# Optimization experiments

Measured on AMD Instinct MI355X. Metric: run time of the kernel, lower is better.

Reference implementation:

```python
import jax, jax.numpy as jnp
import numpy as np
from jax import lax

# shifts generated by _generate_shifts(kernel_size=3): (s1, s2) pairs with
# (s1, s2) >= (0, 0) lexicographically, excluding (0, 0)
SHIFTS = [(0, 1), (1, -1), (1, 0), (1, 1)]


def conv2d_same(x, w, b):
    # x: (B, C_in, H, W), w: (C_out, C_in, kH, kW), b: (C_out,)
    y = lax.conv_general_dilated(
        x, w, window_strides=(1, 1), padding='SAME',
        dimension_numbers=('NCHW', 'OIHW', 'NCHW'))
    return y + b[None, :, None, None]


def setup_inputs() -> dict:
    key = jax.random.key(0)
    k1, k2, k3, k4, k5 = jax.random.split(key, 5)
    B, C_in, C_out, H, W, K = 8, 64, 64, 256, 256, 3
    fan = C_in * K * K
    return {
        'x': jax.random.normal(k1, (B, C_in, H, W), dtype=jnp.float32),
        'w1': jax.random.normal(k2, (C_out, C_in, K, K), dtype=jnp.float32) / np.sqrt(fan),
        'b1': jax.random.normal(k3, (C_out,), dtype=jnp.float32) * 0.01,
        'w2': jax.random.normal(k4, (C_out, C_in, K, K), dtype=jnp.float32) / np.sqrt(fan),
        'b2': jax.random.normal(k5, (C_out,), dtype=jnp.float32) * 0.01,
    }


def reference(x, w1, b1, w2, b2):
    linear_term = conv2d_same(x, w1, b1)
    # torch.roll(x, shifts=(shift_y, shift_x), dims=(2,3)) with
    # circular_shift(x, s1, s2) -> shift_x=s1, shift_y=s2.
    # conv2 is linear, so sum_i conv2(prod_i) == conv2(sum_i prod_i)
    # with the bias added once per shift.
    quad_in = jnp.zeros_like(x)
    for s1, s2 in SHIFTS:
        x_shifted = jnp.roll(x, shift=(s2, s1), axis=(2, 3))
        quad_in = quad_in + jnp.clip(x * x_shifted, -1.0, 1.0)
    quadratic_term = conv2d_same(quad_in, w2, b2 * float(len(SHIFTS)))
    return linear_term + quadratic_term
```

## Files before the change

kernel.cpp:

```cpp
#include <hip/hip_runtime.h>
#include <stdint.h>


typedef short s16x8 __attribute__((ext_vector_type(8)));
typedef float f32x4 __attribute__((ext_vector_type(4)));

__device__ __forceinline__ float clip1(float v) { return fminf(fmaxf(v, -1.f), 1.f); }

__device__ __forceinline__ unsigned short f2bf(float f) {
    union { float f; unsigned u; } v; v.f = f;
    unsigned u = v.u;
    return (unsigned short)((u + 0x7fffu + ((u >> 16) & 1u)) >> 16);
}

__device__ __forceinline__ float bf2f(unsigned short u) {
    union { unsigned v; float f; } t; t.v = ((unsigned)u) << 16; return t.f;
}

__global__ void prep_w(const float* __restrict__ w1, const float* __restrict__ w2,
                       unsigned short* __restrict__ Wb) {
    int idx = blockIdx.x * 256 + threadIdx.x;
    int kk = idx % 96;
    int rest = idx / 96;
    int co = rest & 63; rest >>= 6;
    int cc = rest & 3;
    int kh = rest >> 2;
    int kw = kk >> 5;
    int cci = kk & 31;
    int c2 = cc * 32 + cci;
    const float* src = (c2 < 64) ? w1 : w2;
    int ci = c2 & 63;
    Wb[idx] = f2bf(src[((co * 64 + ci) * 3 + kh) * 3 + kw]);
}

__global__ __launch_bounds__(512, 1) void prep_u2(const float* __restrict__ x,
                                                  unsigned short* __restrict__ U) {
    __shared__ unsigned short X[3][64][268];
    int bid = blockIdx.x;
    int bh = ((bid & 7) << 8) + (bid >> 3);
    int b = bh >> 8, h = bh & 255;
    int tid = threadIdx.x;

    for (int it = 0; it < 24; ++it) {
        int idx = tid + (it << 9);
        int w4 = idx & 63;
        int c  = (idx >> 6) & 63;
        int r  = idx >> 12;
        int gr = (h + r + 255) & 255;
        const float4 v = *(const float4*)(x + (((size_t)(b * 64 + c)) << 16)
                                            + (gr << 8) + (w4 << 2));
        ushort4 p;
        p.x = f2bf(v.x); p.y = f2bf(v.y); p.z = f2bf(v.z); p.w = f2bf(v.w);
        *(ushort4*)&X[r][c][w4 << 2] = p;
    }
    __syncthreads();

    int c  = tid & 63;
    int wv = tid >> 6;
    int p0 = wv << 5;
    int pm0 = (p0 + 255) & 255;
    float pxc = bf2f(X[1][c][pm0]);
    float pxu = bf2f(X[0][c][pm0]);
    float pxd = bf2f(X[2][c][pm0]);
    size_t base = ((size_t)bh) << 8;
#pragma unroll 4
    for (int i = 0; i < 32; ++i) {
        int p = p0 + i;
        unsigned short xcb = X[1][c][p];
        float xc = bf2f(xcb);
        float xu = bf2f(X[0][c][p]);
        float xd = bf2f(X[2][c][p]);
        float q = clip1(xc * xu) + clip1(xc * pxd) + clip1(xc * pxc) + clip1(xc * pxu);
        size_t po = (base + p) << 7;
        U[po + c]      = xcb;
        U[po + 64 + c] = f2bf(q);
        pxc = xc; pxu = xu; pxd = xd;
    }
}

__global__ __launch_bounds__(1024, 2) void conv4(
        const unsigned short* __restrict__ U,
        const unsigned short* __restrict__ Wb,
        const float* __restrict__ b1, const float* __restrict__ b2,
        float* __restrict__ out) {
    __shared__ unsigned short Alds[3][64][104];
    __shared__ unsigned short Ib[2][258][40];

    int bid = blockIdx.x;
    int logical = ((bid & 7) << 6) + (bid >> 3);
    int b = logical >> 6;
    int h0 = (logical & 63) << 2;
    int tid = threadIdx.x;
    int wid = tid >> 6;
    int ln = tid & 63;
    int lr = ln & 15;
    int lq = ln >> 4;
    int rowsel = wid >> 2;
    int pq = wid & 3;
    int o = h0 + rowsel;

    f32x4 acc[4][4];
#pragma unroll
    for (int m = 0; m < 4; m++)
#pragma unroll
        for (int n = 0; n < 4; n++) {
            acc[m][n][0] = 0.f; acc[m][n][1] = 0.f; acc[m][n][2] = 0.f; acc[m][n][3] = 0.f;
        }

    const size_t ubase = ((size_t)b) << 23;

    int cur = 0;
    for (int cc = 0; cc < 4; cc++) {
        for (int i = tid; i < 2304; i += 1024) {
            int kh = i / 768;
            int rem = i - kh * 768;
            int co = rem / 12;
            int kk = (rem - co * 12) << 3;
            *(uint4*)&Alds[kh][co][kk] =
                *(const uint4*)&Wb[(((size_t)((kh * 4 + cc) * 64 + co)) * 96) + kk];
        }
        {
            int r = h0 - 1;
            if (r >= 0) {
                const unsigned short* usrc = U + ubase + (((size_t)r) << 15) + cc * 32;
                for (int i = tid; i < 1032; i += 1024) {
                    int p = i >> 2, q = i & 3;
                    uint4 v = (p == 0 || p == 257) ? make_uint4(0u, 0u, 0u, 0u)
                                                   : *(const uint4*)&usrc[(((size_t)(p - 1)) << 7) + q * 8];
                    *(uint4*)&Ib[cur][p][q * 8] = v;
                }
            }
        }
        __syncthreads();

        for (int j = 0; j < 6; j++) {
            int rn = h0 + j;
            bool have = (j < 5) && (rn <= 255);
            uint4 s0;
            int i0 = tid;
            if (have) {
                const unsigned short* usrc = U + ubase + (((size_t)rn) << 15) + cc * 32;
                int p = i0 >> 2, q = i0 & 3;
                s0 = (p == 0) ? make_uint4(0u, 0u, 0u, 0u)
                              : *(const uint4*)&usrc[(((size_t)(p - 1)) << 7) + q * 8];
            }
            int r = h0 - 1 + j;
            int kh = j - rowsel;
            if (kh >= 0 && kh <= 2 && r >= 0 && r <= 255) {
#pragma unroll
                for (int kw = 0; kw < 3; kw++) {
                    s16x8 af[4], bfr[4];
#pragma unroll
                    for (int m = 0; m < 4; m++)
                        af[m] = *(const s16x8*)&Alds[kh][m * 16 + lr][kw * 32 + lq * 8];
#pragma unroll
                    for (int n = 0; n < 4; n++)
                        bfr[n] = *(const s16x8*)&Ib[cur][(pq << 6) + n * 16 + lr + kw][lq * 8];
#pragma unroll
                    for (int m = 0; m < 4; m++)
#pragma unroll
                        for (int n = 0; n < 4; n++)
                            acc[m][n] = __builtin_amdgcn_mfma_f32_16x16x32_bf16(af[m], bfr[n], acc[m][n], 0, 0, 0);
                }
            }
            if (have) {
                { int p = i0 >> 2, q = i0 & 3; *(uint4*)&Ib[cur ^ 1][p][q * 8] = s0; }
                if (tid < 8) {
                    int i2 = tid + 1024;
                    int p = i2 >> 2, q = i2 & 3;
                    const unsigned short* usrc = U + ubase + (((size_t)rn) << 15) + cc * 32;
                    uint4 v = (p == 257) ? make_uint4(0u, 0u, 0u, 0u)
                                         : *(const uint4*)&usrc[(((size_t)(p - 1)) << 7) + q * 8];
                    *(uint4*)&Ib[cur ^ 1][p][q * 8] = v;
                }
            }
            __syncthreads();
            if (j < 5) cur ^= 1;
        }
    }

#pragma unroll
    for (int m = 0; m < 4; m++) {
#pragma unroll
        for (int jj = 0; jj < 4; jj++) {
            int co = m * 16 + lq * 4 + jj;
            float bias = b1[co] + 4.f * b2[co];
#pragma unroll
            for (int n = 0; n < 4; n++) {
                int wpix = (pq << 6) + n * 16 + lr;
                out[(((size_t)(b * 64 + co)) << 16) + (o << 8) + wpix] = acc[m][n][jj] + bias;
            }
        }
    }
}

__global__ void fallback_conv(const float* __restrict__ x,
                              const float* __restrict__ w1, const float* __restrict__ b1,
                              const float* __restrict__ w2, const float* __restrict__ b2,
                              float* __restrict__ out) {
    size_t idx = (size_t)blockIdx.x * 256 + threadIdx.x;
    int w = idx & 255;
    int h = (int)(idx >> 8) & 255;
    int co = (int)(idx >> 16) & 63;
    int b = (int)(idx >> 22);
    float acc = b1[co] + 4.f * b2[co];
    const float* xb = x + (((size_t)b * 64) << 16);
    for (int ci = 0; ci < 64; ci++) {
        const float* xp = xb + (((size_t)ci) << 16);
        for (int kh = 0; kh < 3; kh++) {
            int hh = h + kh - 1;
            if (hh < 0 || hh > 255) continue;
            for (int kw = 0; kw < 3; kw++) {
                int ww = w + kw - 1;
                if (ww < 0 || ww > 255) continue;
                float xv = xp[(hh << 8) + ww];
                float g1 = w1[((co * 64 + ci) * 3 + kh) * 3 + kw];
                float g2 = w2[((co * 64 + ci) * 3 + kh) * 3 + kw];
                int hm = (hh + 255) & 255, hp = (hh + 1) & 255, wm = (ww + 255) & 255;
                float q = clip1(xv * xp[(hm << 8) + ww]) + clip1(xv * xp[(hp << 8) + wm])
                        + clip1(xv * xp[(hh << 8) + wm]) + clip1(xv * xp[(hm << 8) + wm]);
                acc = fmaf(g1, xv, acc);
                acc = fmaf(g2, q, acc);
            }
        }
    }
    out[idx] = acc;
}

extern "C" void kernel_launch(void* const* d_in, const int* in_sizes, int n_in,
                              void* d_out, int out_size, void* d_ws, size_t ws_size,
                              hipStream_t stream) {
    const float* x  = (const float*)d_in[0];
    const float* w1 = (const float*)d_in[1];
    const float* b1 = (const float*)d_in[2];
    const float* w2 = (const float*)d_in[3];
    const float* b2 = (const float*)d_in[4];
    float* out = (float*)d_out;

    const size_t WB_BYTES = 262144;
    const size_t U_BYTES  = (size_t)8 * 256 * 256 * 128 * 2;
    if (ws_size >= WB_BYTES + U_BYTES) {
        unsigned short* Wb = (unsigned short*)d_ws;
        unsigned short* U  = (unsigned short*)((char*)d_ws + WB_BYTES);
        prep_w<<<dim3(288), dim3(256), 0, stream>>>(w1, w2, Wb);
        prep_u2<<<dim3(2048), dim3(512), 0, stream>>>(x, U);
        conv4<<<dim3(512), dim3(1024), 0, stream>>>(U, Wb, b1, b2, out);
    } else {
        fallback_conv<<<dim3(131072), dim3(256), 0, stream>>>(x, w1, b1, w2, b2, out);
    }
}
```

Before: 190.8 us.

## Split conv tiles into width halves with 512-thread blocks and MFMA priority

The conv kernel now tiles each 4-row band into two 128-column halves, so it launches 1024 blocks of 512 threads instead of 512 blocks of 1024. The input row buffer in LDS is halved and halo columns are handled through global column bounds checks. The aim is to raise occupancy and scheduling flexibility, with more blocks per CU and less LDS per block. It also raises wave priority around the MFMA section. The cost is more redundant weight loads into LDS (per block, per channel chunk) and extra halo column loads.

```diff
diff --git a/kernel.cpp b/kernel.cpp
--- a/kernel.cpp
+++ b/kernel.cpp
@@ -78,25 +78,28 @@
     }
 }
 
-__global__ __launch_bounds__(1024, 2) void conv4(
+__global__ __launch_bounds__(512, 4) void conv5(
         const unsigned short* __restrict__ U,
         const unsigned short* __restrict__ Wb,
         const float* __restrict__ b1, const float* __restrict__ b2,
         float* __restrict__ out) {
     __shared__ unsigned short Alds[3][64][104];
-    __shared__ unsigned short Ib[2][258][40];
+    __shared__ unsigned short Ib[2][130][40];
 
     int bid = blockIdx.x;
-    int logical = ((bid & 7) << 6) + (bid >> 3);
-    int b = logical >> 6;
-    int h0 = (logical & 63) << 2;
+    int logical = ((bid & 7) << 7) + (bid >> 3);
+    int b = logical >> 7;
+    int rem = logical & 127;
+    int h0 = (rem >> 1) << 2;
+    int whalf = rem & 1;
+    int w0 = whalf << 7;
     int tid = threadIdx.x;
     int wid = tid >> 6;
     int ln = tid & 63;
     int lr = ln & 15;
     int lq = ln >> 4;
-    int rowsel = wid >> 2;
-    int pq = wid & 3;
+    int rowsel = wid >> 1;
+    int pq = wid & 1;
     int o = h0 + rowsel;
 
     f32x4 acc[4][4];
@@ -111,11 +114,11 @@
 
     int cur = 0;
     for (int cc = 0; cc < 4; cc++) {
-        for (int i = tid; i < 2304; i += 1024) {
+        for (int i = tid; i < 2304; i += 512) {
             int kh = i / 768;
-            int rem = i - kh * 768;
-            int co = rem / 12;
-            int kk = (rem - co * 12) << 3;
+            int remw = i - kh * 768;
+            int co = remw / 12;
+            int kk = (remw - co * 12) << 3;
             *(uint4*)&Alds[kh][co][kk] =
                 *(const uint4*)&Wb[(((size_t)((kh * 4 + cc) * 64 + co)) * 96) + kk];
         }
@@ -123,10 +126,11 @@
             int r = h0 - 1;
             if (r >= 0) {
                 const unsigned short* usrc = U + ubase + (((size_t)r) << 15) + cc * 32;
-                for (int i = tid; i < 1032; i += 1024) {
+                for (int i = tid; i < 520; i += 512) {
                     int p = i >> 2, q = i & 3;
-                    uint4 v = (p == 0 || p == 257) ? make_uint4(0u, 0u, 0u, 0u)
-                                                   : *(const uint4*)&usrc[(((size_t)(p - 1)) << 7) + q * 8];
+                    int gcol = w0 + p - 1;
+                    uint4 v = (gcol < 0 || gcol > 255) ? make_uint4(0u, 0u, 0u, 0u)
+                              : *(const uint4*)&usrc[(((size_t)gcol) << 7) + q * 8];
                     *(uint4*)&Ib[cur][p][q * 8] = v;
                 }
             }
@@ -137,16 +141,17 @@
             int rn = h0 + j;
             bool have = (j < 5) && (rn <= 255);
             uint4 s0;
-            int i0 = tid;
             if (have) {
                 const unsigned short* usrc = U + ubase + (((size_t)rn) << 15) + cc * 32;
-                int p = i0 >> 2, q = i0 & 3;
-                s0 = (p == 0) ? make_uint4(0u, 0u, 0u, 0u)
-                              : *(const uint4*)&usrc[(((size_t)(p - 1)) << 7) + q * 8];
+                int p = tid >> 2, q = tid & 3;
+                int gcol = w0 + p - 1;
+                s0 = (gcol < 0 || gcol > 255) ? make_uint4(0u, 0u, 0u, 0u)
+                     : *(const uint4*)&usrc[(((size_t)gcol) << 7) + q * 8];
             }
             int r = h0 - 1 + j;
             int kh = j - rowsel;
             if (kh >= 0 && kh <= 2 && r >= 0 && r <= 255) {
+                __builtin_amdgcn_s_setprio(1);
 #pragma unroll
                 for (int kw = 0; kw < 3; kw++) {
                     s16x8 af[4], bfr[4];
@@ -162,15 +167,17 @@
                         for (int n = 0; n < 4; n++)
                             acc[m][n] = __builtin_amdgcn_mfma_f32_16x16x32_bf16(af[m], bfr[n], acc[m][n], 0, 0, 0);
                 }
+                __builtin_amdgcn_s_setprio(0);
             }
             if (have) {
-                { int p = i0 >> 2, q = i0 & 3; *(uint4*)&Ib[cur ^ 1][p][q * 8] = s0; }
+                { int p = tid >> 2, q = tid & 3; *(uint4*)&Ib[cur ^ 1][p][q * 8] = s0; }
                 if (tid < 8) {
-                    int i2 = tid + 1024;
+                    int i2 = tid + 512;
                     int p = i2 >> 2, q = i2 & 3;
+                    int gcol = w0 + p - 1;
                     const unsigned short* usrc = U + ubase + (((size_t)rn) << 15) + cc * 32;
-                    uint4 v = (p == 257) ? make_uint4(0u, 0u, 0u, 0u)
-                                         : *(const uint4*)&usrc[(((size_t)(p - 1)) << 7) + q * 8];
+                    uint4 v = (gcol < 0 || gcol > 255) ? make_uint4(0u, 0u, 0u, 0u)
+                              : *(const uint4*)&usrc[(((size_t)gcol) << 7) + q * 8];
                     *(uint4*)&Ib[cur ^ 1][p][q * 8] = v;
                 }
             }
@@ -187,7 +194,7 @@
             float bias = b1[co] + 4.f * b2[co];
 #pragma unroll
             for (int n = 0; n < 4; n++) {
-                int wpix = (pq << 6) + n * 16 + lr;
+                int wpix = w0 + (pq << 6) + n * 16 + lr;
                 out[(((size_t)(b * 64 + co)) << 16) + (o << 8) + wpix] = acc[m][n][jj] + bias;
             }
         }
@@ -244,7 +251,7 @@
         unsigned short* U  = (unsigned short*)((char*)d_ws + WB_BYTES);
         prep_w<<<dim3(288), dim3(256), 0, stream>>>(w1, w2, Wb);
         prep_u2<<<dim3(2048), dim3(512), 0, stream>>>(x, U);
-        conv4<<<dim3(512), dim3(1024), 0, stream>>>(U, Wb, b1, b2, out);
+        conv5<<<dim3(1024), dim3(512), 0, stream>>>(U, Wb, b1, b2, out);
     } else {
         fallback_conv<<<dim3(131072), dim3(256), 0, stream>>>(x, w1, b1, w2, b2, out);
     }
```

After: 165.0 us. 1.16x faster.
